# Kernel tuning notes

Hardware: AMD Instinct MI355X
Metric: run time of the kernel (lower is better)

The kernel has to match this reference:

```python
import jax, jax.numpy as jnp
import numpy as np

N_HEADS = 16
CHUNK = 64        # attention_chunk_size
WINDOW = 256      # local_attention_size


def combined_sliding_chunkwise_allowed(seq_len, chunk, window):
    """Boolean [S,S] mask, True = attention allowed.
    Full (non-causal) attention within each chunk, plus a sliding window of
    `window` keys ending just before the query's chunk start."""
    qi = jnp.arange(seq_len)[:, None]   # query index
    kj = jnp.arange(seq_len)[None, :]   # key index
    qc = qi // chunk                    # query chunk id
    kc = kj // chunk                    # key chunk id
    same_chunk = kc == qc
    in_window = (kj >= qi - window + 1) & (kj < qc * chunk)
    return same_chunk | in_window


def setup_inputs() -> dict:
    key = jax.random.key(0)
    kq, kk, kv = jax.random.split(key, 3)
    B, N, E = 4, 2048, 512
    return {
        "q": jax.random.normal(kq, (B, N, E), dtype=jnp.float32),
        "k": jax.random.normal(kk, (B, N, E), dtype=jnp.float32),
        "v": jax.random.normal(kv, (B, N, E), dtype=jnp.float32),
        "cache_index": 0,
    }


def reference(q, k, v, cache_index):
    B, N, E = q.shape
    h = N_HEADS
    d = E // h
    # 'bs n (h d) -> bs h n d'
    qh = q.reshape(B, N, h, d).transpose(0, 2, 1, 3)
    kh = k.reshape(B, N, h, d).transpose(0, 2, 1, 3)
    vh = v.reshape(B, N, h, d).transpose(0, 2, 1, 3)
    # max_cache_size == 0: full_k/full_v are just k/v; mask over full key len
    allowed = combined_sliding_chunkwise_allowed(N, CHUNK, WINDOW)  # [S,S]
    scale = 1.0 / jnp.sqrt(jnp.asarray(d, dtype=qh.dtype))
    scores = jnp.einsum("bhqd,bhkd->bhqk", qh, kh) * scale
    scores = jnp.where(allowed, scores, -jnp.inf)
    probs = jax.nn.softmax(scores, axis=-1)
    out = jnp.einsum("bhqk,bhkd->bhqd", probs, vh)
    # 'bs h n d -> bs n (h d)'
    return out.transpose(0, 2, 1, 3).reshape(B, N, E)
```

## Files before the change

kernel.cpp:

```cpp
#include <hip/hip_runtime.h>
#include <hip/hip_bf16.h>

#define NB 4
#define NH 16
#define SEQ 2048
#define EMB 512
#define DH 32
#define CHUNKQ 64
#define WIN 256

typedef __attribute__((ext_vector_type(8))) short short8;
typedef __attribute__((ext_vector_type(4))) float f32x4;

__device__ __forceinline__ unsigned cvt_pk_bf16(float lo, float hi) {
    unsigned r;
    asm("v_cvt_pk_bf16_f32 %0, %1, %2" : "=v"(r) : "v"(lo), "v"(hi));
    return r;
}


__global__ __launch_bounds__(256, 3)
void attn_chunk_kernel(const float* __restrict__ q, const float* __restrict__ k,
                       const float* __restrict__ v, float* __restrict__ out)
{
    constexpr int KSTR = 40;
    constexpr int VSTR = 328;
    constexpr int PSTR = 20;
    __shared__ __align__(16) ushort Ks[320 * KSTR];
    __shared__ __align__(16) ushort Vt[32 * VSTR];
    __shared__ __align__(16) unsigned Pbuf[4][16 * PSTR];

    const unsigned bid = (blockIdx.x & 7) * 256 + (blockIdx.x >> 3);
    const int cid = bid & 31;
    const int h   = (bid >> 5) & 15;
    const int b   = bid >> 9;
    const int q0  = cid * CHUNKQ;
    const int hi  = q0 + CHUNKQ;
    const int kstart = (hi - 320 > 0) ? (hi - 320) : 0;
    const int KT  = hi - kstart;

    const int tid = threadIdx.x;
    const int e4  = (tid & 7) * 4;
    const int r0  = tid >> 3;
    const int d2  = (tid & 15) * 2;
    const int kp  = tid >> 4;

    float4 fk[10];
    float2 va[10], vb[10];
    #pragma unroll
    for (int it = 0; it < 10; ++it) {
        const size_t kbase = (size_t)(b * SEQ + kstart + r0 + it * 32) * EMB + h * DH + e4;
        fk[it] = *(const float4*)(k + kbase);
        const size_t vbase = (size_t)(b * SEQ + kstart + 32 * it + 2 * kp) * EMB + h * DH + d2;
        va[it] = *(const float2*)(v + vbase);
        vb[it] = *(const float2*)(v + vbase + EMB);
    }

    const int w   = tid >> 6;
    const int l   = tid & 63;
    const int l16 = l & 15;
    const int kg  = l >> 4;
    const int k0  = kg * 8;

    const float* qrow = q + ((size_t)(b * SEQ + q0 + 16 * w + l16) * EMB + h * DH + k0);
    const float4 qa = *(const float4*)qrow;
    const float4 qc = *(const float4*)(qrow + 4);
    union { short8 s; unsigned u[4]; } qb;
    qb.u[0] = cvt_pk_bf16(qa.x, qa.y);
    qb.u[1] = cvt_pk_bf16(qa.z, qa.w);
    qb.u[2] = cvt_pk_bf16(qc.x, qc.y);
    qb.u[3] = cvt_pk_bf16(qc.z, qc.w);

    #pragma unroll
    for (int it = 0; it < 10; ++it) {
        uint2 kw;
        kw.x = cvt_pk_bf16(fk[it].x, fk[it].y);
        kw.y = cvt_pk_bf16(fk[it].z, fk[it].w);
        *(uint2*)(Ks + (r0 + it * 32) * KSTR + e4) = kw;
        *(unsigned*)(Vt + (d2 + 0) * VSTR + 32 * it + 2 * kp) = cvt_pk_bf16(va[it].x, vb[it].x);
        *(unsigned*)(Vt + (d2 + 1) * VSTR + 32 * it + 2 * kp) = cvt_pk_bf16(va[it].y, vb[it].y);
    }
    __syncthreads();

    const float scale = 0.17677669529663687f;
    const int   iq    = q0 + 16 * w + l16;
    const int   lowk  = iq - (WIN - 1);
    unsigned* pw = &Pbuf[w][l16 * PSTR];

    const f32x4 zero = {0.f, 0.f, 0.f, 0.f};
    f32x4 o0 = zero, o1 = zero;
    float srow = 0.f;

    #pragma unroll
    for (int t = 0; t < 10; ++t) {
        if (t * 32 < KT) {
            const short8 ka = *(const short8*)(Ks + (32 * t + l16) * KSTR + k0);
            const short8 kb = *(const short8*)(Ks + (32 * t + 16 + l16) * KSTR + k0);
            f32x4 s_lo = __builtin_amdgcn_mfma_f32_16x16x32_bf16(ka, qb.s, zero, 0, 0, 0);
            f32x4 s_hi = __builtin_amdgcn_mfma_f32_16x16x32_bf16(kb, qb.s, zero, 0, 0, 0);

            const int kk = kstart + 32 * t + 4 * kg;
            float p[8];
            #pragma unroll
            for (int r = 0; r < 4; ++r) {
                p[r]     = (kk + r      >= lowk) ? __expf(s_lo[r] * scale) : 0.f;
                p[r + 4] = (kk + r + 16 >= lowk) ? __expf(s_hi[r] * scale) : 0.f;
            }
            srow += ((p[0] + p[1]) + (p[2] + p[3])) + ((p[4] + p[5]) + (p[6] + p[7]));

            uint2 wlo, whi;
            wlo.x = cvt_pk_bf16(p[0], p[1]);  wlo.y = cvt_pk_bf16(p[2], p[3]);
            whi.x = cvt_pk_bf16(p[4], p[5]);  whi.y = cvt_pk_bf16(p[6], p[7]);
            *(uint2*)(pw + 2 * kg)     = wlo;
            *(uint2*)(pw + 8 + 2 * kg) = whi;
            const short8 pa = *(const short8*)(pw + 4 * kg);

            const short8 bv0 = *(const short8*)(Vt + l16 * VSTR + 32 * t + k0);
            const short8 bv1 = *(const short8*)(Vt + (16 + l16) * VSTR + 32 * t + k0);
            o0 = __builtin_amdgcn_mfma_f32_16x16x32_bf16(pa, bv0, o0, 0, 0, 0);
            o1 = __builtin_amdgcn_mfma_f32_16x16x32_bf16(pa, bv1, o1, 0, 0, 0);
        }
    }

    srow += __shfl_xor(srow, 16);
    srow += __shfl_xor(srow, 32);
    #pragma unroll
    for (int r = 0; r < 4; ++r) {
        const float sq  = __shfl(srow, 4 * kg + r);
        const float inv = 1.0f / sq;
        float* dst = out + (size_t)(b * SEQ + q0 + 16 * w + 4 * kg + r) * EMB + h * DH;
        dst[l16]      = o0[r] * inv;
        dst[16 + l16] = o1[r] * inv;
    }
}

extern "C" void kernel_launch(void* const* d_in, const int* in_sizes, int n_in,
                              void* d_out, int out_size, void* d_ws, size_t ws_size,
                              hipStream_t stream) {
    const float* q = (const float*)d_in[0];
    const float* k = (const float*)d_in[1];
    const float* v = (const float*)d_in[2];
    float* out = (float*)d_out;
    const int grid = NB * NH * (SEQ / CHUNKQ);
    attn_chunk_kernel<<<grid, 256, 0, stream>>>(q, k, v, out);
}
```

Before: 26.44 us.

## Process two adjacent query chunks per block to share K/V tile loads

Each block now handles a pair of consecutive 64-query chunks, loading a 384-key K/V window once and reusing it for both chunks instead of loading 320 keys per chunk. This cuts redundant global K/V traffic and the bf16 conversion work. The grid is halved to 1024 blocks, occupancy hints drop from 3 to 2, and LDS use and register pressure rise, which may reduce latency hiding.

Result: slower. 29.90 us (+13.1%).

```diff
diff --git a/kernel.cpp b/kernel.cpp
--- a/kernel.cpp
+++ b/kernel.cpp
@@ -6,7 +6,6 @@
 #define SEQ 2048
 #define EMB 512
 #define DH 32
-#define CHUNKQ 64
 #define WIN 256
 
 typedef __attribute__((ext_vector_type(8))) short short8;
@@ -19,25 +18,30 @@
 }
 
 
-__global__ __launch_bounds__(256, 3)
+__global__ __launch_bounds__(256, 2)
 void attn_chunk_kernel(const float* __restrict__ q, const float* __restrict__ k,
                        const float* __restrict__ v, float* __restrict__ out)
 {
-    constexpr int KSTR = 40;
-    constexpr int VSTR = 328;
+    constexpr int KSTR = 36;
+    constexpr int VSTR = 392;
     constexpr int PSTR = 20;
-    __shared__ __align__(16) ushort Ks[320 * KSTR];
+    __shared__ __align__(16) ushort Ks[384 * KSTR];
     __shared__ __align__(16) ushort Vt[32 * VSTR];
-    __shared__ __align__(16) unsigned Pbuf[4][16 * PSTR];
+    __shared__ __align__(16) unsigned Pbuf[8][16 * PSTR];
 
-    const unsigned bid = (blockIdx.x & 7) * 256 + (blockIdx.x >> 3);
-    const int cid = bid & 31;
-    const int h   = (bid >> 5) & 15;
-    const int b   = bid >> 9;
-    const int q0  = cid * CHUNKQ;
-    const int hi  = q0 + CHUNKQ;
-    const int kstart = (hi - 320 > 0) ? (hi - 320) : 0;
-    const int KT  = hi - kstart;
+    const unsigned bid = (blockIdx.x & 7) * 128 + (blockIdx.x >> 3);
+    const int cp = bid & 15;
+    const int h  = (bid >> 4) & 15;
+    const int b  = bid >> 8;
+    const int q0A = cp * 128;
+    const int q0B = q0A + 64;
+    const int hiA = q0A + 64;
+    const int hiB = q0B + 64;
+    const int base = (q0A - 256 > 0) ? (q0A - 256) : 0;
+    const int KTA  = hiA - base;
+    const int kstartB = (hiB - 320 > 0) ? (hiB - 320) : 0;
+    const int offB = kstartB - base;
+    const int KTB  = hiB - kstartB;
 
     const int tid = threadIdx.x;
     const int e4  = (tid & 7) * 4;
@@ -45,13 +49,13 @@
     const int d2  = (tid & 15) * 2;
     const int kp  = tid >> 4;
 
-    float4 fk[10];
-    float2 va[10], vb[10];
+    float4 fk[12];
+    float2 va[12], vb[12];
     #pragma unroll
-    for (int it = 0; it < 10; ++it) {
-        const size_t kbase = (size_t)(b * SEQ + kstart + r0 + it * 32) * EMB + h * DH + e4;
+    for (int it = 0; it < 12; ++it) {
+        const size_t kbase = (size_t)(b * SEQ + base + r0 + it * 32) * EMB + h * DH + e4;
         fk[it] = *(const float4*)(k + kbase);
-        const size_t vbase = (size_t)(b * SEQ + kstart + 32 * it + 2 * kp) * EMB + h * DH + d2;
+        const size_t vbase = (size_t)(b * SEQ + base + 32 * it + 2 * kp) * EMB + h * DH + d2;
         va[it] = *(const float2*)(v + vbase);
         vb[it] = *(const float2*)(v + vbase + EMB);
     }
@@ -62,17 +66,24 @@
     const int kg  = l >> 4;
     const int k0  = kg * 8;
 
-    const float* qrow = q + ((size_t)(b * SEQ + q0 + 16 * w + l16) * EMB + h * DH + k0);
-    const float4 qa = *(const float4*)qrow;
-    const float4 qc = *(const float4*)(qrow + 4);
-    union { short8 s; unsigned u[4]; } qb;
-    qb.u[0] = cvt_pk_bf16(qa.x, qa.y);
-    qb.u[1] = cvt_pk_bf16(qa.z, qa.w);
-    qb.u[2] = cvt_pk_bf16(qc.x, qc.y);
-    qb.u[3] = cvt_pk_bf16(qc.z, qc.w);
+    const float* qrowA = q + ((size_t)(b * SEQ + q0A + 16 * w + l16) * EMB + h * DH + k0);
+    const float* qrowB = q + ((size_t)(b * SEQ + q0B + 16 * w + l16) * EMB + h * DH + k0);
+    const float4 qa1 = *(const float4*)qrowA;
+    const float4 qa2 = *(const float4*)(qrowA + 4);
+    const float4 qb1 = *(const float4*)qrowB;
+    const float4 qb2 = *(const float4*)(qrowB + 4);
+    union { short8 s; unsigned u[4]; } qfA, qfB;
+    qfA.u[0] = cvt_pk_bf16(qa1.x, qa1.y);
+    qfA.u[1] = cvt_pk_bf16(qa1.z, qa1.w);
+    qfA.u[2] = cvt_pk_bf16(qa2.x, qa2.y);
+    qfA.u[3] = cvt_pk_bf16(qa2.z, qa2.w);
+    qfB.u[0] = cvt_pk_bf16(qb1.x, qb1.y);
+    qfB.u[1] = cvt_pk_bf16(qb1.z, qb1.w);
+    qfB.u[2] = cvt_pk_bf16(qb2.x, qb2.y);
+    qfB.u[3] = cvt_pk_bf16(qb2.z, qb2.w);
 
     #pragma unroll
-    for (int it = 0; it < 10; ++it) {
+    for (int it = 0; it < 12; ++it) {
         uint2 kw;
         kw.x = cvt_pk_bf16(fk[it].x, fk[it].y);
         kw.y = cvt_pk_bf16(fk[it].z, fk[it].w);
@@ -83,54 +94,85 @@
     __syncthreads();
 
     const float scale = 0.17677669529663687f;
-    const int   iq    = q0 + 16 * w + l16;
-    const int   lowk  = iq - (WIN - 1);
-    unsigned* pw = &Pbuf[w][l16 * PSTR];
+    const int iqA   = q0A + 16 * w + l16;
+    const int iqB   = q0B + 16 * w + l16;
+    const int lowkA = iqA - (WIN - 1);
+    const int lowkB = iqB - (WIN - 1);
+    unsigned* pwA = &Pbuf[2 * w + 0][l16 * PSTR];
+    unsigned* pwB = &Pbuf[2 * w + 1][l16 * PSTR];
 
     const f32x4 zero = {0.f, 0.f, 0.f, 0.f};
-    f32x4 o0 = zero, o1 = zero;
-    float srow = 0.f;
+    f32x4 o0A = zero, o1A = zero, o0B = zero, o1B = zero;
+    float srowA = 0.f, srowB = 0.f;
 
     #pragma unroll
     for (int t = 0; t < 10; ++t) {
-        if (t * 32 < KT) {
+        if (t * 32 < KTA) {
             const short8 ka = *(const short8*)(Ks + (32 * t + l16) * KSTR + k0);
             const short8 kb = *(const short8*)(Ks + (32 * t + 16 + l16) * KSTR + k0);
-            f32x4 s_lo = __builtin_amdgcn_mfma_f32_16x16x32_bf16(ka, qb.s, zero, 0, 0, 0);
-            f32x4 s_hi = __builtin_amdgcn_mfma_f32_16x16x32_bf16(kb, qb.s, zero, 0, 0, 0);
-
-            const int kk = kstart + 32 * t + 4 * kg;
+            f32x4 s_lo = __builtin_amdgcn_mfma_f32_16x16x32_bf16(ka, qfA.s, zero, 0, 0, 0);
+            f32x4 s_hi = __builtin_amdgcn_mfma_f32_16x16x32_bf16(kb, qfA.s, zero, 0, 0, 0);
+            const int kk = base + 32 * t + 4 * kg;
             float p[8];
             #pragma unroll
             for (int r = 0; r < 4; ++r) {
-                p[r]     = (kk + r      >= lowk) ? __expf(s_lo[r] * scale) : 0.f;
-                p[r + 4] = (kk + r + 16 >= lowk) ? __expf(s_hi[r] * scale) : 0.f;
+                p[r]     = (kk + r      >= lowkA) ? __expf(s_lo[r] * scale) : 0.f;
+                p[r + 4] = (kk + r + 16 >= lowkA) ? __expf(s_hi[r] * scale) : 0.f;
             }
-            srow += ((p[0] + p[1]) + (p[2] + p[3])) + ((p[4] + p[5]) + (p[6] + p[7]));
-
+            srowA += ((p[0] + p[1]) + (p[2] + p[3])) + ((p[4] + p[5]) + (p[6] + p[7]));
             uint2 wlo, whi;
             wlo.x = cvt_pk_bf16(p[0], p[1]);  wlo.y = cvt_pk_bf16(p[2], p[3]);
             whi.x = cvt_pk_bf16(p[4], p[5]);  whi.y = cvt_pk_bf16(p[6], p[7]);
-            *(uint2*)(pw + 2 * kg)     = wlo;
-            *(uint2*)(pw + 8 + 2 * kg) = whi;
-            const short8 pa = *(const short8*)(pw + 4 * kg);
-
+            *(uint2*)(pwA + 2 * kg)     = wlo;
+            *(uint2*)(pwA + 8 + 2 * kg) = whi;
+            const short8 pa = *(const short8*)(pwA + 4 * kg);
             const short8 bv0 = *(const short8*)(Vt + l16 * VSTR + 32 * t + k0);
             const short8 bv1 = *(const short8*)(Vt + (16 + l16) * VSTR + 32 * t + k0);
-            o0 = __builtin_amdgcn_mfma_f32_16x16x32_bf16(pa, bv0, o0, 0, 0, 0);
-            o1 = __builtin_amdgcn_mfma_f32_16x16x32_bf16(pa, bv1, o1, 0, 0, 0);
+            o0A = __builtin_amdgcn_mfma_f32_16x16x32_bf16(pa, bv0, o0A, 0, 0, 0);
+            o1A = __builtin_amdgcn_mfma_f32_16x16x32_bf16(pa, bv1, o1A, 0, 0, 0);
+        }
+        if (t * 32 < KTB) {
+            const short8 ka = *(const short8*)(Ks + (offB + 32 * t + l16) * KSTR + k0);
+            const short8 kb = *(const short8*)(Ks + (offB + 32 * t + 16 + l16) * KSTR + k0);
+            f32x4 s_lo = __builtin_amdgcn_mfma_f32_16x16x32_bf16(ka, qfB.s, zero, 0, 0, 0);
+            f32x4 s_hi = __builtin_amdgcn_mfma_f32_16x16x32_bf16(kb, qfB.s, zero, 0, 0, 0);
+            const int kk = kstartB + 32 * t + 4 * kg;
+            float p[8];
+            #pragma unroll
+            for (int r = 0; r < 4; ++r) {
+                p[r]     = (kk + r      >= lowkB) ? __expf(s_lo[r] * scale) : 0.f;
+                p[r + 4] = (kk + r + 16 >= lowkB) ? __expf(s_hi[r] * scale) : 0.f;
+            }
+            srowB += ((p[0] + p[1]) + (p[2] + p[3])) + ((p[4] + p[5]) + (p[6] + p[7]));
+            uint2 wlo, whi;
+            wlo.x = cvt_pk_bf16(p[0], p[1]);  wlo.y = cvt_pk_bf16(p[2], p[3]);
+            whi.x = cvt_pk_bf16(p[4], p[5]);  whi.y = cvt_pk_bf16(p[6], p[7]);
+            *(uint2*)(pwB + 2 * kg)     = wlo;
+            *(uint2*)(pwB + 8 + 2 * kg) = whi;
+            const short8 pa = *(const short8*)(pwB + 4 * kg);
+            const short8 bv0 = *(const short8*)(Vt + l16 * VSTR + offB + 32 * t + k0);
+            const short8 bv1 = *(const short8*)(Vt + (16 + l16) * VSTR + offB + 32 * t + k0);
+            o0B = __builtin_amdgcn_mfma_f32_16x16x32_bf16(pa, bv0, o0B, 0, 0, 0);
+            o1B = __builtin_amdgcn_mfma_f32_16x16x32_bf16(pa, bv1, o1B, 0, 0, 0);
         }
     }
 
-    srow += __shfl_xor(srow, 16);
-    srow += __shfl_xor(srow, 32);
+    srowA += __shfl_xor(srowA, 16);
+    srowA += __shfl_xor(srowA, 32);
+    srowB += __shfl_xor(srowB, 16);
+    srowB += __shfl_xor(srowB, 32);
     #pragma unroll
     for (int r = 0; r < 4; ++r) {
-        const float sq  = __shfl(srow, 4 * kg + r);
-        const float inv = 1.0f / sq;
-        float* dst = out + (size_t)(b * SEQ + q0 + 16 * w + 4 * kg + r) * EMB + h * DH;
-        dst[l16]      = o0[r] * inv;
-        dst[16 + l16] = o1[r] * inv;
+        const float sqA = __shfl(srowA, 4 * kg + r);
+        const float invA = 1.0f / sqA;
+        float* dstA = out + (size_t)(b * SEQ + q0A + 16 * w + 4 * kg + r) * EMB + h * DH;
+        dstA[l16]      = o0A[r] * invA;
+        dstA[16 + l16] = o1A[r] * invA;
+        const float sqB = __shfl(srowB, 4 * kg + r);
+        const float invB = 1.0f / sqB;
+        float* dstB = out + (size_t)(b * SEQ + q0B + 16 * w + 4 * kg + r) * EMB + h * DH;
+        dstB[l16]      = o0B[r] * invB;
+        dstB[16 + l16] = o1B[r] * invB;
     }
 }
 
@@ -141,6 +183,6 @@
     const float* k = (const float*)d_in[1];
     const float* v = (const float*)d_in[2];
     float* out = (float*)d_out;
-    const int grid = NB * NH * (SEQ / CHUNKQ);
+    const int grid = NB * NH * (SEQ / 128);
     attn_chunk_kernel<<<grid, 256, 0, stream>>>(q, k, v, out);
 }
```

## Load K fragments directly from global into registers, dropping LDS staging

Applied to the files above, without the earlier changes.

Removes the shared-memory K tile and its bf16 conversion pass. Each wave now loads its K fragments from global memory straight into MFMA operand layout, prefetching the next 32-key tile one iteration ahead, and converts them to bf16 in registers. This cuts LDS usage and staging stores, and the launch bound is raised to ask for 4 blocks per CU. The cost is that every wave re-reads the full K window, so K traffic is 4x redundant (relying on L2), and load latency may be exposed inside the loop.

After: 54.30 us. +105.4%, slower.

```diff
diff --git a/kernel.cpp b/kernel.cpp
--- a/kernel.cpp
+++ b/kernel.cpp
@@ -19,14 +19,12 @@
 }
 
 
-__global__ __launch_bounds__(256, 3)
+__global__ __launch_bounds__(256, 4)
 void attn_chunk_kernel(const float* __restrict__ q, const float* __restrict__ k,
                        const float* __restrict__ v, float* __restrict__ out)
 {
-    constexpr int KSTR = 40;
     constexpr int VSTR = 328;
     constexpr int PSTR = 20;
-    __shared__ __align__(16) ushort Ks[320 * KSTR];
     __shared__ __align__(16) ushort Vt[32 * VSTR];
     __shared__ __align__(16) unsigned Pbuf[4][16 * PSTR];
 
@@ -40,17 +38,12 @@
     const int KT  = hi - kstart;
 
     const int tid = threadIdx.x;
-    const int e4  = (tid & 7) * 4;
-    const int r0  = tid >> 3;
     const int d2  = (tid & 15) * 2;
     const int kp  = tid >> 4;
 
-    float4 fk[10];
     float2 va[10], vb[10];
     #pragma unroll
     for (int it = 0; it < 10; ++it) {
-        const size_t kbase = (size_t)(b * SEQ + kstart + r0 + it * 32) * EMB + h * DH + e4;
-        fk[it] = *(const float4*)(k + kbase);
         const size_t vbase = (size_t)(b * SEQ + kstart + 32 * it + 2 * kp) * EMB + h * DH + d2;
         va[it] = *(const float2*)(v + vbase);
         vb[it] = *(const float2*)(v + vbase + EMB);
@@ -73,13 +66,17 @@
 
     #pragma unroll
     for (int it = 0; it < 10; ++it) {
-        uint2 kw;
-        kw.x = cvt_pk_bf16(fk[it].x, fk[it].y);
-        kw.y = cvt_pk_bf16(fk[it].z, fk[it].w);
-        *(uint2*)(Ks + (r0 + it * 32) * KSTR + e4) = kw;
         *(unsigned*)(Vt + (d2 + 0) * VSTR + 32 * it + 2 * kp) = cvt_pk_bf16(va[it].x, vb[it].x);
         *(unsigned*)(Vt + (d2 + 1) * VSTR + 32 * it + 2 * kp) = cvt_pk_bf16(va[it].y, vb[it].y);
     }
+
+    const float* kbase_lo = k + ((size_t)(b * SEQ + kstart + l16) * EMB + h * DH + k0);
+    const float* kbase_hi = kbase_lo + (size_t)16 * EMB;
+    float4 ka0 = *(const float4*)(kbase_lo);
+    float4 ka1 = *(const float4*)(kbase_lo + 4);
+    float4 kb0 = *(const float4*)(kbase_hi);
+    float4 kb1 = *(const float4*)(kbase_hi + 4);
+
     __syncthreads();
 
     const float scale = 0.17677669529663687f;
@@ -94,10 +91,27 @@
     #pragma unroll
     for (int t = 0; t < 10; ++t) {
         if (t * 32 < KT) {
-            const short8 ka = *(const short8*)(Ks + (32 * t + l16) * KSTR + k0);
-            const short8 kb = *(const short8*)(Ks + (32 * t + 16 + l16) * KSTR + k0);
-            f32x4 s_lo = __builtin_amdgcn_mfma_f32_16x16x32_bf16(ka, qb.s, zero, 0, 0, 0);
-            f32x4 s_hi = __builtin_amdgcn_mfma_f32_16x16x32_bf16(kb, qb.s, zero, 0, 0, 0);
+            union { short8 s; unsigned u[4]; } kaf, kbf;
+            kaf.u[0] = cvt_pk_bf16(ka0.x, ka0.y);
+            kaf.u[1] = cvt_pk_bf16(ka0.z, ka0.w);
+            kaf.u[2] = cvt_pk_bf16(ka1.x, ka1.y);
+            kaf.u[3] = cvt_pk_bf16(ka1.z, ka1.w);
+            kbf.u[0] = cvt_pk_bf16(kb0.x, kb0.y);
+            kbf.u[1] = cvt_pk_bf16(kb0.z, kb0.w);
+            kbf.u[2] = cvt_pk_bf16(kb1.x, kb1.y);
+            kbf.u[3] = cvt_pk_bf16(kb1.z, kb1.w);
+
+            if (t < 9) {
+                const float* pl = kbase_lo + (size_t)(t + 1) * 32 * EMB;
+                const float* ph = kbase_hi + (size_t)(t + 1) * 32 * EMB;
+                ka0 = *(const float4*)(pl);
+                ka1 = *(const float4*)(pl + 4);
+                kb0 = *(const float4*)(ph);
+                kb1 = *(const float4*)(ph + 4);
+            }
+
+            f32x4 s_lo = __builtin_amdgcn_mfma_f32_16x16x32_bf16(kaf.s, qb.s, zero, 0, 0, 0);
+            f32x4 s_hi = __builtin_amdgcn_mfma_f32_16x16x32_bf16(kbf.s, qb.s, zero, 0, 0, 0);
 
             const int kk = kstart + 32 * t + 4 * kg;
             float p[8];
```

## Split key range in two blocks per chunk and combine partials

Applied to the files above, without the earlier changes.

Each query chunk's key range is split across two thread blocks, so twice as many blocks each run with half the shared memory and can reach higher occupancy. Each block writes its unnormalized partial output and row sums to workspace, and a second kernel adds the two halves and normalizes. Because there is no running max, the partials can simply be added. The cost is an extra launch plus a workspace write and read, and the original kernel remains as a fallback when the workspace is too small.

Result: slower. 33.73 us (+27.6%).

```diff
diff --git a/kernel.cpp b/kernel.cpp
--- a/kernel.cpp
+++ b/kernel.cpp
@@ -16,6 +16,159 @@
     unsigned r;
     asm("v_cvt_pk_bf16_f32 %0, %1, %2" : "=v"(r) : "v"(lo), "v"(hi));
     return r;
+}
+
+
+__global__ __launch_bounds__(256, 5)
+void attn_split_kernel(const float* __restrict__ q, const float* __restrict__ k,
+                       const float* __restrict__ v, float* __restrict__ part)
+{
+    constexpr int KSTR = 36;
+    constexpr int VSTR = 168;
+    constexpr int PSTR = 20;
+    __shared__ __align__(16) ushort Ks[160 * KSTR];
+    __shared__ __align__(16) ushort Vt[32 * VSTR];
+    __shared__ __align__(16) unsigned Pbuf[4][16 * PSTR];
+
+    const unsigned bid = (blockIdx.x & 7) * 512 + (blockIdx.x >> 3);
+    const int s    = bid & 1;
+    const int task = bid >> 1;
+    const int cid  = task & 31;
+    const int h    = (task >> 5) & 15;
+    const int b    = task >> 9;
+    const int q0   = cid * CHUNKQ;
+    const int hi   = q0 + CHUNKQ;
+    const int kstart = (hi - 320 > 0) ? (hi - 320) : 0;
+    const int KT   = hi - kstart;
+    const int half = KT >> 1;
+    const int ks0  = kstart + s * half;
+
+    const int tid = threadIdx.x;
+    const int e4  = (tid & 7) * 4;
+    const int r0  = tid >> 3;
+    const int d2  = (tid & 15) * 2;
+    const int kp  = tid >> 4;
+
+    float4 fk[5];
+    float2 va[5], vb[5];
+    #pragma unroll
+    for (int it = 0; it < 5; ++it) {
+        const size_t kbase = (size_t)(b * SEQ + ks0 + r0 + it * 32) * EMB + h * DH + e4;
+        fk[it] = *(const float4*)(k + kbase);
+        const size_t vbase = (size_t)(b * SEQ + ks0 + 32 * it + 2 * kp) * EMB + h * DH + d2;
+        va[it] = *(const float2*)(v + vbase);
+        vb[it] = *(const float2*)(v + vbase + EMB);
+    }
+
+    const int w   = tid >> 6;
+    const int l   = tid & 63;
+    const int l16 = l & 15;
+    const int kg  = l >> 4;
+    const int k0  = kg * 8;
+
+    const float* qrow = q + ((size_t)(b * SEQ + q0 + 16 * w + l16) * EMB + h * DH + k0);
+    const float4 qa = *(const float4*)qrow;
+    const float4 qc = *(const float4*)(qrow + 4);
+    union { short8 s8; unsigned u[4]; } qb;
+    qb.u[0] = cvt_pk_bf16(qa.x, qa.y);
+    qb.u[1] = cvt_pk_bf16(qa.z, qa.w);
+    qb.u[2] = cvt_pk_bf16(qc.x, qc.y);
+    qb.u[3] = cvt_pk_bf16(qc.z, qc.w);
+
+    #pragma unroll
+    for (int it = 0; it < 5; ++it) {
+        uint2 kw;
+        kw.x = cvt_pk_bf16(fk[it].x, fk[it].y);
+        kw.y = cvt_pk_bf16(fk[it].z, fk[it].w);
+        *(uint2*)(Ks + (r0 + it * 32) * KSTR + e4) = kw;
+        *(unsigned*)(Vt + (d2 + 0) * VSTR + 32 * it + 2 * kp) = cvt_pk_bf16(va[it].x, vb[it].x);
+        *(unsigned*)(Vt + (d2 + 1) * VSTR + 32 * it + 2 * kp) = cvt_pk_bf16(va[it].y, vb[it].y);
+    }
+    __syncthreads();
+
+    const float scale = 0.17677669529663687f;
+    const int   iq    = q0 + 16 * w + l16;
+    const int   lowk  = iq - (WIN - 1);
+    unsigned* pw = &Pbuf[w][l16 * PSTR];
+
+    const f32x4 zero = {0.f, 0.f, 0.f, 0.f};
+    f32x4 o0 = zero, o1 = zero;
+    float srow = 0.f;
+
+    #pragma unroll
+    for (int t = 0; t < 5; ++t) {
+        if (t * 32 < half) {
+            const short8 ka = *(const short8*)(Ks + (32 * t + l16) * KSTR + k0);
+            const short8 kb = *(const short8*)(Ks + (32 * t + 16 + l16) * KSTR + k0);
+            f32x4 s_lo = __builtin_amdgcn_mfma_f32_16x16x32_bf16(ka, qb.s8, zero, 0, 0, 0);
+            f32x4 s_hi = __builtin_amdgcn_mfma_f32_16x16x32_bf16(kb, qb.s8, zero, 0, 0, 0);
+
+            const int kk = ks0 + 32 * t + 4 * kg;
+            float p[8];
+            #pragma unroll
+            for (int r = 0; r < 4; ++r) {
+                p[r]     = (kk + r      >= lowk) ? __expf(s_lo[r] * scale) : 0.f;
+                p[r + 4] = (kk + r + 16 >= lowk) ? __expf(s_hi[r] * scale) : 0.f;
+            }
+            srow += ((p[0] + p[1]) + (p[2] + p[3])) + ((p[4] + p[5]) + (p[6] + p[7]));
+
+            uint2 wlo, whi;
+            wlo.x = cvt_pk_bf16(p[0], p[1]);  wlo.y = cvt_pk_bf16(p[2], p[3]);
+            whi.x = cvt_pk_bf16(p[4], p[5]);  whi.y = cvt_pk_bf16(p[6], p[7]);
+            *(uint2*)(pw + 2 * kg)     = wlo;
+            *(uint2*)(pw + 8 + 2 * kg) = whi;
+            const short8 pa = *(const short8*)(pw + 4 * kg);
+
+            const short8 bv0 = *(const short8*)(Vt + l16 * VSTR + 32 * t + k0);
+            const short8 bv1 = *(const short8*)(Vt + (16 + l16) * VSTR + 32 * t + k0);
+            o0 = __builtin_amdgcn_mfma_f32_16x16x32_bf16(pa, bv0, o0, 0, 0, 0);
+            o1 = __builtin_amdgcn_mfma_f32_16x16x32_bf16(pa, bv1, o1, 0, 0, 0);
+        }
+    }
+
+    float* P = part + (size_t)bid * 2112;
+    #pragma unroll
+    for (int r = 0; r < 4; ++r) {
+        const int row = 16 * w + 4 * kg + r;
+        P[row * 32 + l16]      = o0[r];
+        P[row * 32 + 16 + l16] = o1[r];
+    }
+    srow += __shfl_xor(srow, 16);
+    srow += __shfl_xor(srow, 32);
+    if (kg == 0) P[2048 + 16 * w + l16] = srow;
+}
+
+__global__ __launch_bounds__(256, 8)
+void attn_combine_kernel(const float* __restrict__ part, float* __restrict__ out)
+{
+    const int task = blockIdx.x;
+    const int cid  = task & 31;
+    const int h    = (task >> 5) & 15;
+    const int b    = task >> 9;
+    const int q0   = cid * CHUNKQ;
+
+    const float* A = part + (size_t)(task * 2) * 2112;
+    const float* B = A + 2112;
+
+    const int t  = threadIdx.x;
+    const int qr = t >> 2;
+    const int d8 = (t & 3) * 8;
+
+    const float inv = 1.0f / (A[2048 + qr] + B[2048 + qr]);
+    const float4 a0 = *(const float4*)(A + qr * 32 + d8);
+    const float4 a1 = *(const float4*)(A + qr * 32 + d8 + 4);
+    const float4 b0 = *(const float4*)(B + qr * 32 + d8);
+    const float4 b1 = *(const float4*)(B + qr * 32 + d8 + 4);
+
+    float4 r0, r1;
+    r0.x = (a0.x + b0.x) * inv;  r0.y = (a0.y + b0.y) * inv;
+    r0.z = (a0.z + b0.z) * inv;  r0.w = (a0.w + b0.w) * inv;
+    r1.x = (a1.x + b1.x) * inv;  r1.y = (a1.y + b1.y) * inv;
+    r1.z = (a1.z + b1.z) * inv;  r1.w = (a1.w + b1.w) * inv;
+
+    float* dst = out + (size_t)(b * SEQ + q0 + qr) * EMB + h * DH + d8;
+    *(float4*)dst       = r0;
+    *(float4*)(dst + 4) = r1;
 }
 
 
@@ -141,6 +294,13 @@
     const float* k = (const float*)d_in[1];
     const float* v = (const float*)d_in[2];
     float* out = (float*)d_out;
-    const int grid = NB * NH * (SEQ / CHUNKQ);
-    attn_chunk_kernel<<<grid, 256, 0, stream>>>(q, k, v, out);
-}
+
+    const size_t ws_needed = (size_t)4096 * 2112 * sizeof(float);
+    if (ws_size >= ws_needed) {
+        float* part = (float*)d_ws;
+        attn_split_kernel<<<4096, 256, 0, stream>>>(q, k, v, part);
+        attn_combine_kernel<<<2048, 256, 0, stream>>>(part, out);
+    } else {
+        attn_chunk_kernel<<<NB * NH * (SEQ / CHUNKQ), 256, 0, stream>>>(q, k, v, out);
+    }
+}
```
